# Kernel optimization log

Hardware: AMD Instinct MI355X
Metric: run time of the kernel (lower is better)

## Reference

```python
import jax, jax.numpy as jnp
import numpy as np

T, B, DIM, N = 2048, 16, 1024, 64
INIT_BETA_BIAS = 2.0
EPS = 1e-6


def setup_inputs() -> dict:
    key = jax.random.key(0)
    ks = jax.random.split(key, 6)
    xavier = np.sqrt(2.0 / (N + DIM)).astype(np.float32)
    return {
        "x": jax.random.normal(ks[0], (T, B, DIM), dtype=jnp.float32),
        "S0": jnp.zeros((B, N, N), dtype=jnp.float32),
        "W_k": jax.random.normal(ks[1], (N, DIM), dtype=jnp.float32) * xavier,
        "W_v": jax.random.normal(ks[2], (N, DIM), dtype=jnp.float32) * xavier,
        "W_q": jax.random.normal(ks[3], (N, DIM), dtype=jnp.float32) * xavier,
        "W_beta": jax.random.normal(ks[4], (N, DIM), dtype=jnp.float32) * xavier,
        "b_beta": jnp.full((N,), INIT_BETA_BIAS, dtype=jnp.float32),
    }


def reference(x, S0, W_k, W_v, W_q, W_beta, b_beta):
    # Batched projections: [T, B, dim] @ [dim, n] -> [T, B, n]
    k_all = jnp.einsum("tbd,nd->tbn", x, W_k)
    v_all = jnp.einsum("tbd,nd->tbn", x, W_v)
    q_all = jnp.einsum("tbd,nd->tbn", x, W_q)
    g_all = jax.nn.sigmoid(jnp.einsum("tbd,nd->tbn", x, W_beta) + b_beta)

    def step(S, inp):
        k, v, q, g = inp  # each [B, n]
        k_norm = k / (jnp.linalg.norm(k, axis=-1, keepdims=True) + EPS)
        retrieved = jnp.einsum("bij,bj->bi", S, k_norm)
        delta = v - retrieved
        S_new = g[:, :, None] * S + delta[:, :, None] * k_norm[:, None, :]
        Sq = jnp.einsum("bij,bj->bi", S_new, q)
        out = Sq * jax.nn.silu(Sq)  # self-gated output
        return S_new, out

    S_final, output = jax.lax.scan(step, S0, (k_all, v_all, q_all, g_all))
    return output, S_final
```

## Files before the change

kernel.cpp:

```cpp
#include <hip/hip_runtime.h>
#include <math.h>

#define T_STEPS 2048
#define BATCH   16
#define DIM     1024
#define NSTATE  64
#define NFIELD  256
#define PROJ_TSTRIDE (BATCH * NFIELD)
static constexpr float EPS = 1e-6f;

#define AS1 __attribute__((address_space(1)))
#define AS3 __attribute__((address_space(3)))

typedef _Float16 f16x8 __attribute__((ext_vector_type(8)));
typedef _Float16 f16x4 __attribute__((ext_vector_type(4)));
typedef float    f32x4 __attribute__((ext_vector_type(4)));

template <int CTRL>
__device__ __forceinline__ float dpp_add(float x) {
    int yi = __builtin_amdgcn_update_dpp(0, __float_as_int(x), CTRL, 0xF, 0xF, true);
    return x + __int_as_float(yi);
}
__device__ __forceinline__ float xor16_add(float x) {
    int y = __builtin_amdgcn_ds_swizzle(__float_as_int(x), 0x401F);
    return x + __int_as_float(y);
}
__device__ __forceinline__ float reduce32(float x) {
    x = dpp_add<0x121>(x); x = dpp_add<0x122>(x);
    x = dpp_add<0x124>(x); x = dpp_add<0x128>(x);
    return xor16_add(x);
}
__device__ __forceinline__ void reduce32x2(float& x, float& y) {
    x = dpp_add<0x121>(x); y = dpp_add<0x121>(y);
    x = dpp_add<0x122>(x); y = dpp_add<0x122>(y);
    x = dpp_add<0x124>(x); y = dpp_add<0x124>(y);
    x = dpp_add<0x128>(x); y = dpp_add<0x128>(y);
    x = xor16_add(x);      y = xor16_add(y);
}
__device__ __forceinline__ void reduce32x3(float& x, float& y, float& z) {
    x = dpp_add<0x121>(x); y = dpp_add<0x121>(y); z = dpp_add<0x121>(z);
    x = dpp_add<0x122>(x); y = dpp_add<0x122>(y); z = dpp_add<0x122>(z);
    x = dpp_add<0x124>(x); y = dpp_add<0x124>(y); z = dpp_add<0x124>(z);
    x = dpp_add<0x128>(x); y = dpp_add<0x128>(y); z = dpp_add<0x128>(z);
    x = xor16_add(x);      y = xor16_add(y);      z = xor16_add(z);
}
__device__ __forceinline__ void reduce16x2(float& x, float& y) {
    x = dpp_add<0x121>(x); y = dpp_add<0x121>(y);
    x = dpp_add<0x122>(x); y = dpp_add<0x122>(y);
    x = dpp_add<0x124>(x); y = dpp_add<0x124>(y);
    x = dpp_add<0x128>(x); y = dpp_add<0x128>(y);
}
__device__ __forceinline__ float dotp(const float4& u, const float4& w) {
    float t0 = u.x * w.x; t0 = fmaf(u.y, w.y, t0);
    float t1 = u.z * w.z; t1 = fmaf(u.w, w.w, t1);
    return t0 + t1;
}
__device__ __forceinline__ float dotp2(const float2& u, const float2& w) {
    return fmaf(u.y, w.y, u.x * w.x);
}


#define PBM   128
#define KSTEP 64
#define NKS   (DIM / KSTEP)

__global__ __launch_bounds__(256) void prep_w16(
    const float* __restrict__ Wk, const float* __restrict__ Wv,
    const float* __restrict__ Wq, const float* __restrict__ Wb,
    _Float16* __restrict__ W16)
{
    const int flat = blockIdx.x * 256 + threadIdx.x;
    const int lane = flat & 63;
    const int st   = (flat >> 6) & 31;
    const int ks   = flat >> 11;
    const int cg = st & 15, kc2 = st >> 4;
    const int col = cg * 16 + (lane & 15);
    const int field = col >> 6, wrow = col & 63;
    const float* Wf = (field == 0 ? Wk : field == 1 ? Wv : field == 2 ? Wq : Wb);
    const float* src = Wf + (size_t)wrow * DIM + ks * 64 + kc2 * 32 + (lane >> 4) * 8;
    const float4 a = *(const float4*)(src);
    const float4 b = *(const float4*)(src + 4);
    f16x8 r;
    r[0] = (_Float16)a.x; r[1] = (_Float16)a.y; r[2] = (_Float16)a.z; r[3] = (_Float16)a.w;
    r[4] = (_Float16)b.x; r[5] = (_Float16)b.y; r[6] = (_Float16)b.z; r[7] = (_Float16)b.w;
    *(f16x8*)(W16 + (size_t)flat * 8) = r;
}

__global__ __launch_bounds__(512, 1) void proj_mfma(
    const float* __restrict__ x, const _Float16* __restrict__ W16,
    const float* __restrict__ bb, float* __restrict__ proj)
{
    __shared__ _Float16 Asub[2][16][64][8];
    __shared__ _Float16 Bsub[2][32][64][8];

    const int tid = threadIdx.x;
    const int w = tid >> 6, wl = tid & 63;
    const int wm = w >> 2, wn = w & 3;
    const int l15 = wl & 15, lr = wl >> 4;
    const size_t mbase = (size_t)blockIdx.x * PBM;

    _Float16* const abase = &Asub[0][0][0][0];
    _Float16* const bbase = &Bsub[0][0][0][0];

    const float* asrc[4];
    int aoff[4];
    #pragma unroll
    for (int it = 0; it < 4; ++it) {
        const int fid = it * 512 + tid;
        const int row = fid >> 4, kq = (fid & 15) * 4;
        asrc[it] = x + (mbase + row) * (size_t)DIM + kq;
        aoff[it] = ((kq >> 5) * 8 + (row >> 4)) * 512
                 + ((row & 15) + ((kq >> 3) & 3) * 16) * 8
                 + (kq & 7);
    }
    const _Float16* bsrc[4];
    int boff[4];
    #pragma unroll
    for (int m = 0; m < 4; ++m) {
        const int st = w * 4 + m;
        bsrc[m] = W16 + ((size_t)st * 64 + wl) * 8;
        boff[m] = st * 512;
    }

    auto stageB = [&](int ks, int buf) {
        #pragma unroll
        for (int m = 0; m < 4; ++m) {
            const _Float16* g = bsrc[m] + (size_t)ks * 16384;
            void* lp = (char*)bbase + (size_t)(buf * 16384 + boff[m]) * 2;
            __builtin_amdgcn_global_load_lds((const AS1 void*)g, (AS3 void*)lp, 16, 0, 0);
        }
    };

    float4 h0[4], h1[4];
    auto loadA = [&](int ks, float4* h) {
        #pragma unroll
        for (int it = 0; it < 4; ++it)
            h[it] = *(const float4*)(asrc[it] + ks * KSTEP);
    };
    auto writeA = [&](const float4* h, int buf) {
        #pragma unroll
        for (int it = 0; it < 4; ++it) {
            f16x4 v;
            v[0] = (_Float16)h[it].x; v[1] = (_Float16)h[it].y;
            v[2] = (_Float16)h[it].z; v[3] = (_Float16)h[it].w;
            *(f16x4*)(abase + buf * 8192 + aoff[it]) = v;
        }
    };

    f32x4 acc[4][4] = {};

    loadA(0, h0);
    stageB(0, 0);
    loadA(1, h1);
    writeA(h0, 0);
    __syncthreads();

    #pragma unroll
    for (int ks = 0; ks < NKS; ++ks) {
        const int buf = ks & 1;
        if (ks + 1 < NKS) stageB(ks + 1, buf ^ 1);
        if (ks + 2 < NKS) loadA(ks + 2, (ks & 1) ? h1 : h0);

        #pragma unroll
        for (int kc = 0; kc < 2; ++kc) {
            f16x8 af[4], bf[4];
            #pragma unroll
            for (int mf = 0; mf < 4; ++mf)
                af[mf] = *(const f16x8*)&Asub[buf][kc * 8 + wm * 4 + mf][wl][0];
            #pragma unroll
            for (int nf = 0; nf < 4; ++nf)
                bf[nf] = *(const f16x8*)&Bsub[buf][kc * 16 + wn * 4 + nf][wl][0];
            #pragma unroll
            for (int mf = 0; mf < 4; ++mf)
                #pragma unroll
                for (int nf = 0; nf < 4; ++nf)
                    acc[mf][nf] = __builtin_amdgcn_mfma_f32_16x16x32_f16(
                        af[mf], bf[nf], acc[mf][nf], 0, 0, 0);
        }

        if (ks + 1 < NKS) writeA((ks & 1) ? h0 : h1, buf ^ 1);
        __syncthreads();
    }

    if (wn == 0) {
        #pragma unroll
        for (int mf = 0; mf < 4; ++mf) {
            f32x4 s = acc[mf][0] * acc[mf][0];
            #pragma unroll
            for (int nf = 1; nf < 4; ++nf) s += acc[mf][nf] * acc[mf][nf];
            #pragma unroll
            for (int r = 0; r < 4; ++r) {
                float t = s[r];
                t += __shfl_xor(t, 1); t += __shfl_xor(t, 2);
                t += __shfl_xor(t, 4); t += __shfl_xor(t, 8);
                const float sc = 1.f / (sqrtf(t) + EPS);
                #pragma unroll
                for (int nf = 0; nf < 4; ++nf) acc[mf][nf][r] *= sc;
            }
        }
    }
    if (wn == 3) {
        #pragma unroll
        for (int nf = 0; nf < 4; ++nf) {
            const float bv = bb[nf * 16 + l15];
            #pragma unroll
            for (int mf = 0; mf < 4; ++mf)
                #pragma unroll
                for (int r = 0; r < 4; ++r)
                    acc[mf][nf][r] = 1.f / (1.f + __expf(-(acc[mf][nf][r] + bv)));
        }
    }

    #pragma unroll
    for (int mf = 0; mf < 4; ++mf)
        #pragma unroll
        for (int r = 0; r < 4; ++r) {
            float* dst = proj + (mbase + wm * 64 + mf * 16 + lr * 4 + r) * NFIELD
                              + wn * 64 + l15;
            dst[0]  = acc[mf][0][r];
            dst[16] = acc[mf][1][r];
            dst[32] = acc[mf][2][r];
            dst[48] = acc[mf][3][r];
        }
}

#define KAP_T 2112

__global__ __launch_bounds__(256) void kappa_kernel(
    const float* __restrict__ proj, float* __restrict__ kap2)
{
    const int tid = threadIdx.x;
    const int gid = blockIdx.x * 16 + (tid >> 4);
    const int l   = tid & 15;
    const int t = gid >> 4, b = gid & 15;
    if (t >= T_STEPS) {
        if (l == 0) *(float2*)(kap2 + (size_t)gid * 2) = make_float2(0.f, 0.f);
        return;
    }
    const float* base = proj + ((size_t)t * BATCH + b) * NFIELD;
    const float4 k0 = *(const float4*)(base + 4 * l);
    const float4 q0 = *(const float4*)(base + 128 + 4 * l);
    float cp = 0.f;
    float cq = dotp(k0, q0);
    if (t + 1 < T_STEPS) {
        const float4 k1 = *(const float4*)(base + PROJ_TSTRIDE + 4 * l);
        cp = dotp(k0, k1);
    }
    reduce16x2(cp, cq);
    if (l == 0) *(float2*)(kap2 + (size_t)gid * 2) = make_float2(cp, cq);
}


#define CH 32
#define NCHUNK (T_STEPS / CH)

__global__ __launch_bounds__(256, 1) void scan_kernel(
    const float* __restrict__ proj,
    const float* __restrict__ kap2,
    const float* __restrict__ S0,
    float* __restrict__ out,
    float* __restrict__ Sfin)
{
    __shared__ float KQ[2][CH][128];
    __shared__ float VG[2][CH][16];
    __shared__ float KP2[2][CH][2];

    const int tid  = threadIdx.x;
    const int w    = tid >> 6;
    const int wl   = tid & 63;
    const int half = wl >> 5;
    const int jl   = wl & 31;
    const int b    = blockIdx.x >> 3;
    const int i0   = (blockIdx.x & 7) * 8;
    const int i    = i0 + 2 * w + half;
    const int c0   = 2 * jl;

    const size_t srow = ((size_t)(b * 64 + i)) * 64 + c0;
    float2 S = *(const float2*)(S0 + srow);

    const float* pb = proj + (size_t)b * NFIELD;

    const int l31  = wl & 31;
    const int kq_f = l31 * 4 + ((l31 >= 16) ? 64 : 0);
    const int kq_s = wl >> 5;
    const int idx  = wl & 15;
    const int vg_f = (idx & 1) ? (192 + i0 + (idx >> 1)) : (64 + i0 + (idx >> 1));
    const int vg_sl = wl >> 4;

    auto stage = [&](int c, int nb) {
        const float* cbase = pb + (size_t)c * CH * PROJ_TSTRIDE;
        #pragma unroll
        for (int m = 0; m < 4; ++m) {
            const int n = w * 4 + m;
            const float* g = cbase + (size_t)(2 * n + kq_s) * PROJ_TSTRIDE + kq_f;
            void* lp = (char*)&KQ[nb][0][0] + n * 1024;
            __builtin_amdgcn_global_load_lds((const AS1 void*)g, (AS3 void*)lp, 16, 0, 0);
        }
        #pragma unroll
        for (int m = 0; m < 2; ++m) {
            const int p = w * 2 + m;
            const float* g = cbase + (size_t)(4 * p + vg_sl) * PROJ_TSTRIDE + vg_f;
            void* lp = (char*)&VG[nb][0][0] + p * 256;
            __builtin_amdgcn_global_load_lds((const AS1 void*)g, (AS3 void*)lp, 4, 0, 0);
        }
        if (w == 0) {
            const float* g = kap2 + ((size_t)(c * CH + (wl >> 1)) * BATCH + b) * 2
                           + (wl & 1);
            void* lp = (char*)&KP2[nb][0][0];
            __builtin_amdgcn_global_load_lds((const AS1 void*)g, (AS3 void*)lp, 4, 0, 0);
        }
    };

    float2 kn_r[4], q_r[4], vg_r[4], kk_r[4];
    const int vgo = 2 * (2 * w + half);

    stage(0, 0);
    __syncthreads();

    float a, cqr, cpr;
    float osel = 0.f;

    for (int c = 0; c < NCHUNK; ++c) {
        const int cb = c & 1;
        const float (*KQc)[128] = KQ[cb];
        const float (*VGc)[16]  = VG[cb];
        const float (*KPc)[2]   = KP2[cb];

        auto ldslot = [&](int s, int j) {
            kn_r[j] = *(const float2*)(&KQc[s][c0]);
            q_r [j] = *(const float2*)(&KQc[s][64 + c0]);
            vg_r[j] = *(const float2*)(&VGc[s][vgo]);
            kk_r[j] = *(const float2*)(&KPc[s][0]);
        };

        #pragma unroll
        for (int j = 0; j < 4; ++j) ldslot(j, j);
        {
            float aP  = dotp2(S, kn_r[0]);
            float cqP = dotp2(S, q_r[0]);
            float cpP = dotp2(S, kn_r[1]);
            reduce32x3(aP, cqP, cpP);
            a = aP; cqr = cqP; cpr = cpP;
        }

        const bool more = (c + 1 < NCHUNK);
        if (more) stage(c + 1, cb ^ 1);

        #pragma unroll
        for (int s = 0; s < CH; ++s) {
            const int j = s & 3;

            const float2 kn = kn_r[j];
            const float  v = vg_r[j].x, g = vg_r[j].y;
            const float2 kk = kk_r[j];

            const float d  = v - a;
            const float sq = fmaf(d, kk.y, g * cqr);
            const float an = fmaf(d, kk.x, g * cpr);

            S.x = fmaf(d, kn.x, g * S.x);
            S.y = fmaf(d, kn.y, g * S.y);

            if (s + 4 < CH) ldslot(s + 4, j);

            if (s + 2 < CH) {
                float cqP = dotp2(S, q_r[(s + 1) & 3]);
                float cpP = dotp2(S, kn_r[(s + 2) & 3]);
                reduce32x2(cpP, cqP);
                cpr = cpP; cqr = cqP;
            } else if (s + 1 < CH) {
                cqr = reduce32(dotp2(S, q_r[(s + 1) & 3]));
            }
            a = an;

            osel = (s == jl) ? sq : osel;
            if (s == CH - 1) {
                const float y = osel * osel / (1.f + __expf(-osel));
                out[((size_t)(c * CH + jl) * BATCH + b) * 64 + i] = y;
            }
        }

        if (more) __syncthreads();
    }

    *(float2*)(Sfin + srow) = S;
}

extern "C" void kernel_launch(void* const* d_in, const int* in_sizes, int n_in,
                              void* d_out, int out_size, void* d_ws, size_t ws_size,
                              hipStream_t stream) {
    const float* x  = (const float*)d_in[0];
    const float* S0 = (const float*)d_in[1];
    const float* Wk = (const float*)d_in[2];
    const float* Wv = (const float*)d_in[3];
    const float* Wq = (const float*)d_in[4];
    const float* Wb = (const float*)d_in[5];
    const float* bb = (const float*)d_in[6];

    float* out  = (float*)d_out;
    float* Sfin = out + (size_t)T_STEPS * BATCH * NSTATE;

    float*    proj = (float*)d_ws;
    float*    kap2 = proj + (size_t)T_STEPS * BATCH * NFIELD;
    _Float16* W16  = (_Float16*)(kap2 + (size_t)KAP_T * BATCH * 2);

    prep_w16<<<128, 256, 0, stream>>>(Wk, Wv, Wq, Wb, W16);
    proj_mfma<<<(T_STEPS * BATCH) / PBM, 512, 0, stream>>>(x, W16, bb, proj);
    kappa_kernel<<<KAP_T, 256, 0, stream>>>(proj, kap2);
    scan_kernel<<<(BATCH * NSTATE) / 8, 256, 0, stream>>>(proj, kap2, S0, out, Sfin);
}
```

Before: 445.7 us.

## Replace per-step serial scan with chunked triangular solve using precomputed Gram matrices

The sequential 32-step inner recurrence, which needed wave reductions every step, is replaced by a chunkwise formulation. A new mn_prep kernel computes masked per-chunk K·K and K·Q Gram matrices, and the scan then solves a triangular system per chunk using broadcast swizzles, cumulative gate products and a single state update per chunk. This shortens the serial dependency chain per timestep and removes the kappa kernel. In exchange it adds a Gram-matrix pass, register pressure (64 Gram values per lane), and possible numerical error from dividing by cumulative gate products that can become small.

```diff
diff --git a/kernel.cpp b/kernel.cpp
--- a/kernel.cpp
+++ b/kernel.cpp
@@ -17,46 +17,15 @@
 typedef float    f32x4 __attribute__((ext_vector_type(4)));
 
 template <int CTRL>
+__device__ __forceinline__ float dpp_pmul(float x) {
+    int yi = __builtin_amdgcn_update_dpp(0x3f800000, __float_as_int(x),
+                                         CTRL, 0xF, 0xF, false);
+    return x * __int_as_float(yi);
+}
+template <int CTRL>
 __device__ __forceinline__ float dpp_add(float x) {
     int yi = __builtin_amdgcn_update_dpp(0, __float_as_int(x), CTRL, 0xF, 0xF, true);
     return x + __int_as_float(yi);
-}
-__device__ __forceinline__ float xor16_add(float x) {
-    int y = __builtin_amdgcn_ds_swizzle(__float_as_int(x), 0x401F);
-    return x + __int_as_float(y);
-}
-__device__ __forceinline__ float reduce32(float x) {
-    x = dpp_add<0x121>(x); x = dpp_add<0x122>(x);
-    x = dpp_add<0x124>(x); x = dpp_add<0x128>(x);
-    return xor16_add(x);
-}
-__device__ __forceinline__ void reduce32x2(float& x, float& y) {
-    x = dpp_add<0x121>(x); y = dpp_add<0x121>(y);
-    x = dpp_add<0x122>(x); y = dpp_add<0x122>(y);
-    x = dpp_add<0x124>(x); y = dpp_add<0x124>(y);
-    x = dpp_add<0x128>(x); y = dpp_add<0x128>(y);
-    x = xor16_add(x);      y = xor16_add(y);
-}
-__device__ __forceinline__ void reduce32x3(float& x, float& y, float& z) {
-    x = dpp_add<0x121>(x); y = dpp_add<0x121>(y); z = dpp_add<0x121>(z);
-    x = dpp_add<0x122>(x); y = dpp_add<0x122>(y); z = dpp_add<0x122>(z);
-    x = dpp_add<0x124>(x); y = dpp_add<0x124>(y); z = dpp_add<0x124>(z);
-    x = dpp_add<0x128>(x); y = dpp_add<0x128>(y); z = dpp_add<0x128>(z);
-    x = xor16_add(x);      y = xor16_add(y);      z = xor16_add(z);
-}
-__device__ __forceinline__ void reduce16x2(float& x, float& y) {
-    x = dpp_add<0x121>(x); y = dpp_add<0x121>(y);
-    x = dpp_add<0x122>(x); y = dpp_add<0x122>(y);
-    x = dpp_add<0x124>(x); y = dpp_add<0x124>(y);
-    x = dpp_add<0x128>(x); y = dpp_add<0x128>(y);
-}
-__device__ __forceinline__ float dotp(const float4& u, const float4& w) {
-    float t0 = u.x * w.x; t0 = fmaf(u.y, w.y, t0);
-    float t1 = u.z * w.z; t1 = fmaf(u.w, w.w, t1);
-    return t0 + t1;
-}
-__device__ __forceinline__ float dotp2(const float2& u, const float2& w) {
-    return fmaf(u.y, w.y, u.x * w.x);
 }
 
 
@@ -224,166 +193,204 @@
         }
 }
 
-#define KAP_T 2112
-
-__global__ __launch_bounds__(256) void kappa_kernel(
-    const float* __restrict__ proj, float* __restrict__ kap2)
-{
-    const int tid = threadIdx.x;
-    const int gid = blockIdx.x * 16 + (tid >> 4);
-    const int l   = tid & 15;
-    const int t = gid >> 4, b = gid & 15;
-    if (t >= T_STEPS) {
-        if (l == 0) *(float2*)(kap2 + (size_t)gid * 2) = make_float2(0.f, 0.f);
-        return;
-    }
-    const float* base = proj + ((size_t)t * BATCH + b) * NFIELD;
-    const float4 k0 = *(const float4*)(base + 4 * l);
-    const float4 q0 = *(const float4*)(base + 128 + 4 * l);
-    float cp = 0.f;
-    float cq = dotp(k0, q0);
-    if (t + 1 < T_STEPS) {
-        const float4 k1 = *(const float4*)(base + PROJ_TSTRIDE + 4 * l);
-        cp = dotp(k0, k1);
-    }
-    reduce16x2(cp, cq);
-    if (l == 0) *(float2*)(kap2 + (size_t)gid * 2) = make_float2(cp, cq);
-}
-
 
 #define CH 32
 #define NCHUNK (T_STEPS / CH)
 
+__global__ __launch_bounds__(256) void mn_prep(
+    const float* __restrict__ proj, float* __restrict__ MN)
+{
+    __shared__ float K[32][68], Q[32][68];
+    const int bch = blockIdx.x;
+    const int b = bch >> 6, ch = bch & 63;
+    const int tid = threadIdx.x;
+
+    {
+        const int t0 = tid >> 3, pp = tid & 7;
+        const float* base = proj + ((size_t)(ch * 32 + t0) * BATCH + b) * NFIELD;
+        *(float4*)&K[t0][8 * pp]     = *(const float4*)(base + 8 * pp);
+        *(float4*)&K[t0][8 * pp + 4] = *(const float4*)(base + 8 * pp + 4);
+        *(float4*)&Q[t0][8 * pp]     = *(const float4*)(base + 128 + 8 * pp);
+        *(float4*)&Q[t0][8 * pp + 4] = *(const float4*)(base + 128 + 8 * pp + 4);
+    }
+    __syncthreads();
+
+    const int t = tid & 31, ub = tid >> 5;
+    float mm[4] = {0.f, 0.f, 0.f, 0.f}, nn[4] = {0.f, 0.f, 0.f, 0.f};
+    #pragma unroll 4
+    for (int db = 0; db < 16; ++db) {
+        const float4 kt = *(const float4*)&K[t][4 * db];
+        #pragma unroll
+        for (int uu = 0; uu < 4; ++uu) {
+            const float4 ku = *(const float4*)&K[ub * 4 + uu][4 * db];
+            const float4 qu = *(const float4*)&Q[ub * 4 + uu][4 * db];
+            mm[uu] = fmaf(kt.x, ku.x, fmaf(kt.y, ku.y,
+                     fmaf(kt.z, ku.z, fmaf(kt.w, ku.w, mm[uu]))));
+            nn[uu] = fmaf(kt.x, qu.x, fmaf(kt.y, qu.y,
+                     fmaf(kt.z, qu.z, fmaf(kt.w, qu.w, nn[uu]))));
+        }
+    }
+    float* dstb = MN + ((size_t)bch * 32) * 64;
+    #pragma unroll
+    for (int uu = 0; uu < 4; ++uu) {
+        const int u = ub * 4 + uu;
+        dstb[(size_t)u * 64 + t]      = (t < u)  ? mm[uu] : 0.f;
+        dstb[(size_t)u * 64 + 32 + t] = (t <= u) ? nn[uu] : 0.f;
+    }
+}
+
+
 __global__ __launch_bounds__(256, 1) void scan_kernel(
     const float* __restrict__ proj,
-    const float* __restrict__ kap2,
+    const float* __restrict__ MN,
     const float* __restrict__ S0,
     float* __restrict__ out,
     float* __restrict__ Sfin)
 {
     __shared__ float KQ[2][CH][128];
-    __shared__ float VG[2][CH][16];
-    __shared__ float KP2[2][CH][2];
+    __shared__ float VGT[2][16][CH];
+    __shared__ float SROW[8][64];
 
     const int tid  = threadIdx.x;
-    const int w    = tid >> 6;
-    const int wl   = tid & 63;
-    const int half = wl >> 5;
-    const int jl   = wl & 31;
+    const int w    = tid >> 6, wl = tid & 63;
+    const int half = wl >> 5, u = wl & 31;
+    const int gid  = 2 * w + half;
     const int b    = blockIdx.x >> 3;
     const int i0   = (blockIdx.x & 7) * 8;
-    const int i    = i0 + 2 * w + half;
-    const int c0   = 2 * jl;
-
-    const size_t srow = ((size_t)(b * 64 + i)) * 64 + c0;
-    float2 S = *(const float2*)(S0 + srow);
+    const int i    = i0 + gid;
+
+    {
+        const float2 s2 = *(const float2*)(S0 + ((size_t)(b * 64 + i)) * 64 + 2 * u);
+        *(float2*)&SROW[gid][2 * u] = s2;
+    }
 
     const float* pb = proj + (size_t)b * NFIELD;
 
-    const int l31  = wl & 31;
-    const int kq_f = l31 * 4 + ((l31 >= 16) ? 64 : 0);
-    const int kq_s = wl >> 5;
-    const int idx  = wl & 15;
-    const int vg_f = (idx & 1) ? (192 + i0 + (idx >> 1)) : (64 + i0 + (idx >> 1));
-    const int vg_sl = wl >> 4;
-
-    auto stage = [&](int c, int nb) {
-        const float* cbase = pb + (size_t)c * CH * PROJ_TSTRIDE;
+    const int l31 = wl & 31;
+    const int glq = wl & 15;
+    const int hlf = (l31 >= 16);
+    auto stage = [&](int c2, int nb) {
+        const float* cbase = pb + (size_t)c2 * CH * PROJ_TSTRIDE;
         #pragma unroll
         for (int m = 0; m < 4; ++m) {
             const int n = w * 4 + m;
-            const float* g = cbase + (size_t)(2 * n + kq_s) * PROJ_TSTRIDE + kq_f;
+            const int s = 2 * n + (wl >> 5);
+            const int field = (hlf ? 128 : 0) + 4 * (glq ^ (s & 7));
+            const float* g = cbase + (size_t)s * PROJ_TSTRIDE + field;
             void* lp = (char*)&KQ[nb][0][0] + n * 1024;
             __builtin_amdgcn_global_load_lds((const AS1 void*)g, (AS3 void*)lp, 16, 0, 0);
         }
         #pragma unroll
         for (int m = 0; m < 2; ++m) {
             const int p = w * 2 + m;
-            const float* g = cbase + (size_t)(4 * p + vg_sl) * PROJ_TSTRIDE + vg_f;
-            void* lp = (char*)&VG[nb][0][0] + p * 256;
+            const int f = 2 * p + (wl >> 5);
+            const int col = wl & 31;
+            const int field = (f < 8) ? (64 + i0 + f) : (192 + i0 + (f - 8));
+            const float* g = cbase + (size_t)col * PROJ_TSTRIDE + field;
+            void* lp = (char*)&VGT[nb][0][0] + p * 256;
             __builtin_amdgcn_global_load_lds((const AS1 void*)g, (AS3 void*)lp, 4, 0, 0);
         }
-        if (w == 0) {
-            const float* g = kap2 + ((size_t)(c * CH + (wl >> 1)) * BATCH + b) * 2
-                           + (wl & 1);
-            void* lp = (char*)&KP2[nb][0][0];
-            __builtin_amdgcn_global_load_lds((const AS1 void*)g, (AS3 void*)lp, 4, 0, 0);
-        }
     };
-
-    float2 kn_r[4], q_r[4], vg_r[4], kk_r[4];
-    const int vgo = 2 * (2 * w + half);
 
     stage(0, 0);
     __syncthreads();
 
-    float a, cqr, cpr;
-    float osel = 0.f;
-
     for (int c = 0; c < NCHUNK; ++c) {
         const int cb = c & 1;
+        if (c + 1 < NCHUNK) stage(c + 1, cb ^ 1);
+
         const float (*KQc)[128] = KQ[cb];
-        const float (*VGc)[16]  = VG[cb];
-        const float (*KPc)[2]   = KP2[cb];
-
-        auto ldslot = [&](int s, int j) {
-            kn_r[j] = *(const float2*)(&KQc[s][c0]);
-            q_r [j] = *(const float2*)(&KQc[s][64 + c0]);
-            vg_r[j] = *(const float2*)(&VGc[s][vgo]);
-            kk_r[j] = *(const float2*)(&KPc[s][0]);
-        };
-
-        #pragma unroll
-        for (int j = 0; j < 4; ++j) ldslot(j, j);
+        const float (*VGTc)[CH] = VGT[cb];
+
+        float Mreg[32], Nreg[32];
         {
-            float aP  = dotp2(S, kn_r[0]);
-            float cqP = dotp2(S, q_r[0]);
-            float cpP = dotp2(S, kn_r[1]);
-            reduce32x3(aP, cqP, cpP);
-            a = aP; cqr = cqP; cpr = cpP;
-        }
-
-        const bool more = (c + 1 < NCHUNK);
-        if (more) stage(c + 1, cb ^ 1);
-
-        #pragma unroll
-        for (int s = 0; s < CH; ++s) {
-            const int j = s & 3;
-
-            const float2 kn = kn_r[j];
-            const float  v = vg_r[j].x, g = vg_r[j].y;
-            const float2 kk = kk_r[j];
-
-            const float d  = v - a;
-            const float sq = fmaf(d, kk.y, g * cqr);
-            const float an = fmaf(d, kk.x, g * cpr);
-
-            S.x = fmaf(d, kn.x, g * S.x);
-            S.y = fmaf(d, kn.y, g * S.y);
-
-            if (s + 4 < CH) ldslot(s + 4, j);
-
-            if (s + 2 < CH) {
-                float cqP = dotp2(S, q_r[(s + 1) & 3]);
-                float cpP = dotp2(S, kn_r[(s + 2) & 3]);
-                reduce32x2(cpP, cqP);
-                cpr = cpP; cqr = cqP;
-            } else if (s + 1 < CH) {
-                cqr = reduce32(dotp2(S, q_r[(s + 1) & 3]));
+            const float* mnb = MN + (((size_t)b * NCHUNK + c) * 32 + u) * 64;
+            #pragma unroll
+            for (int k = 0; k < 8; ++k) {
+                const float4 t4 = *(const float4*)(mnb + 4 * k);
+                Mreg[4 * k] = t4.x; Mreg[4 * k + 1] = t4.y;
+                Mreg[4 * k + 2] = t4.z; Mreg[4 * k + 3] = t4.w;
             }
-            a = an;
-
-            osel = (s == jl) ? sq : osel;
-            if (s == CH - 1) {
-                const float y = osel * osel / (1.f + __expf(-osel));
-                out[((size_t)(c * CH + jl) * BATCH + b) * 64 + i] = y;
+            #pragma unroll
+            for (int k = 0; k < 8; ++k) {
+                const float4 t4 = *(const float4*)(mnb + 32 + 4 * k);
+                Nreg[4 * k] = t4.x; Nreg[4 * k + 1] = t4.y;
+                Nreg[4 * k + 2] = t4.z; Nreg[4 * k + 3] = t4.w;
             }
         }
 
-        if (more) __syncthreads();
-    }
-
-    *(float2*)(Sfin + srow) = S;
+        const float v_u = VGTc[gid][u];
+        const float g_u = VGTc[8 + gid][u];
+        float P = g_u;
+        P = dpp_pmul<0x111>(P);
+        P = dpp_pmul<0x112>(P);
+        P = dpp_pmul<0x114>(P);
+        P = dpp_pmul<0x118>(P);
+        {
+            const int t15 = __builtin_amdgcn_ds_swizzle(__float_as_int(P), (15 << 5));
+            const float pl = __int_as_float(t15);
+            P = (u >= 16) ? P * pl : P;
+        }
+        const float Pm1  = P / g_u;
+        const float invP = 1.0f / P;
+
+        float acc = 0.f, accq = 0.f;
+        #pragma unroll
+        for (int a4 = 0; a4 < 16; ++a4) {
+            const int L = 4 * (a4 ^ (u & 7));
+            const float4 s4 = *(const float4*)&SROW[gid][4 * a4];
+            const float4 k4 = *(const float4*)&KQc[u][L];
+            const float4 q4 = *(const float4*)&KQc[u][64 + L];
+            acc  = fmaf(s4.x, k4.x, fmaf(s4.y, k4.y,
+                   fmaf(s4.z, k4.z, fmaf(s4.w, k4.w, acc))));
+            accq = fmaf(s4.x, q4.x, fmaf(s4.y, q4.y,
+                   fmaf(s4.z, q4.z, fmaf(s4.w, q4.w, accq))));
+        }
+
+        float2 supd = make_float2(0.f, 0.f);
+#define SWEEP_STEP(T)                                                          \
+        {                                                                      \
+            const float e_ = (v_u - Pm1 * acc) * invP;                         \
+            const int ei_ = __builtin_amdgcn_ds_swizzle(__float_as_int(e_),    \
+                                                        ((T) << 5));           \
+            const float eb_ = __int_as_float(ei_);                             \
+            acc  = fmaf(eb_, Mreg[T], acc);                                    \
+            accq = fmaf(eb_, Nreg[T], accq);                                   \
+            const float2 kk_ = *(const float2*)&KQc[T][(2 * u) ^ (4 * ((T) & 7))]; \
+            supd.x = fmaf(eb_, kk_.x, supd.x);                                 \
+            supd.y = fmaf(eb_, kk_.y, supd.y);                                 \
+        }
+        SWEEP_STEP(0)  SWEEP_STEP(1)  SWEEP_STEP(2)  SWEEP_STEP(3)
+        SWEEP_STEP(4)  SWEEP_STEP(5)  SWEEP_STEP(6)  SWEEP_STEP(7)
+        SWEEP_STEP(8)  SWEEP_STEP(9)  SWEEP_STEP(10) SWEEP_STEP(11)
+        SWEEP_STEP(12) SWEEP_STEP(13) SWEEP_STEP(14) SWEEP_STEP(15)
+        SWEEP_STEP(16) SWEEP_STEP(17) SWEEP_STEP(18) SWEEP_STEP(19)
+        SWEEP_STEP(20) SWEEP_STEP(21) SWEEP_STEP(22) SWEEP_STEP(23)
+        SWEEP_STEP(24) SWEEP_STEP(25) SWEEP_STEP(26) SWEEP_STEP(27)
+        SWEEP_STEP(28) SWEEP_STEP(29) SWEEP_STEP(30) SWEEP_STEP(31)
+#undef SWEEP_STEP
+
+        {
+            const int p31 = __builtin_amdgcn_ds_swizzle(__float_as_int(P), (31 << 5));
+            const float Pc = __int_as_float(p31);
+            float2 sold = *(const float2*)&SROW[gid][2 * u];
+            sold.x = Pc * (sold.x + supd.x);
+            sold.y = Pc * (sold.y + supd.y);
+            *(float2*)&SROW[gid][2 * u] = sold;
+        }
+        {
+            const float oq = P * accq;
+            const float y = oq * oq / (1.f + __expf(-oq));
+            out[((size_t)(c * CH + u) * BATCH + b) * 64 + i] = y;
+        }
+
+        __syncthreads();
+    }
+
+    {
+        const float2 sf = *(const float2*)&SROW[gid][2 * u];
+        *(float2*)(Sfin + ((size_t)(b * 64 + i)) * 64 + 2 * u) = sf;
+    }
 }
 
 extern "C" void kernel_launch(void* const* d_in, const int* in_sizes, int n_in,
@@ -401,11 +408,11 @@
     float* Sfin = out + (size_t)T_STEPS * BATCH * NSTATE;
 
     float*    proj = (float*)d_ws;
-    float*    kap2 = proj + (size_t)T_STEPS * BATCH * NFIELD;
-    _Float16* W16  = (_Float16*)(kap2 + (size_t)KAP_T * BATCH * 2);
+    float*    MN   = proj + (size_t)T_STEPS * BATCH * NFIELD;
+    _Float16* W16  = (_Float16*)(MN + (size_t)BATCH * NCHUNK * 32 * 64);
 
     prep_w16<<<128, 256, 0, stream>>>(Wk, Wv, Wq, Wb, W16);
     proj_mfma<<<(T_STEPS * BATCH) / PBM, 512, 0, stream>>>(x, W16, bb, proj);
-    kappa_kernel<<<KAP_T, 256, 0, stream>>>(proj, kap2);
-    scan_kernel<<<(BATCH * NSTATE) / 8, 256, 0, stream>>>(proj, kap2, S0, out, Sfin);
-}
+    mn_prep<<<BATCH * NCHUNK, 256, 0, stream>>>(proj, MN);
+    scan_kernel<<<(BATCH * NSTATE) / 8, 256, 0, stream>>>(proj, MN, S0, out, Sfin);
+}
```

New measurement: 422.0 us. 1.06x faster.
